# Performance work log

Measured on AMD Instinct MI355X. Metric: run time of the kernel, lower is better.

The kernel has to match this reference:

```python
import jax, jax.numpy as jnp
import numpy as np

B, L, H, U = 4, 1024, 16, 64  # batch, length, num_heads, units (per-head dim)
D_IN = 1024                   # input feature dim
D_MODEL = H * U               # 1024


def setup_inputs() -> dict:
    key = jax.random.key(0)
    ks = jax.random.split(key, 12)
    s_in = 1.0 / np.sqrt(D_IN)
    s_md = 1.0 / np.sqrt(D_MODEL)
    return {
        "v": jax.random.normal(ks[0], (B, L, D_IN), jnp.float32),
        "k": jax.random.normal(ks[1], (B, L, D_IN), jnp.float32),
        "q": jax.random.normal(ks[2], (B, L, D_IN), jnp.float32),
        "wq": jax.random.normal(ks[3], (D_IN, D_MODEL), jnp.float32) * s_in,
        "bq": jnp.zeros((D_MODEL,), jnp.float32),
        "wk": jax.random.normal(ks[4], (D_IN, D_MODEL), jnp.float32) * s_in,
        "bk": jnp.zeros((D_MODEL,), jnp.float32),
        "wv": jax.random.normal(ks[5], (D_IN, D_MODEL), jnp.float32) * s_in,
        "bv": jnp.zeros((D_MODEL,), jnp.float32),
        "wo": jax.random.normal(ks[6], (D_MODEL, U), jnp.float32) * s_md,  # dense: units*num_heads -> units
        "bo": jnp.zeros((U,), jnp.float32),
    }


def _split_heads(x):
    # (B, L, H*U) -> (B, H, L, U)
    return x.reshape(B, L, H, U).transpose(0, 2, 1, 3)


def reference(v, k, q, wq, bq, wk, bk, wv, bv, wo, bo):
    qh = _split_heads(q @ wq + bq)
    kh = _split_heads(k @ wk + bk)
    vh = _split_heads(v @ wv + bv)
    scale = 1.0 / jnp.sqrt(jnp.asarray(U, jnp.float32))
    logits = jnp.einsum("bhqd,bhkd->bhqk", qh, kh) * scale
    attn = jax.nn.softmax(logits, axis=-1)  # (B, H, Lq, Lk)
    ctx = jnp.einsum("bhqk,bhkd->bhqd", attn, vh)
    concat = ctx.transpose(0, 2, 1, 3).reshape(B, L, D_MODEL)
    out = concat @ wo + bo  # (B, L, U)
    return out, attn
```

## Files before the change

kernel.cpp:

```cpp
#include <hip/hip_runtime.h>
#include <hip/hip_bf16.h>


typedef __attribute__((ext_vector_type(8))) short s8v;
typedef __attribute__((ext_vector_type(4))) float f4v;

#define MFMA16(a, b, c) __builtin_amdgcn_mfma_f32_16x16x32_bf16(a, b, c, 0, 0, 0)

__device__ __forceinline__ ushort f2bf(float x) {
    unsigned u = __float_as_uint(x);
    return (ushort)((u + 0x7FFF + ((u >> 16) & 1)) >> 16);
}
__device__ __forceinline__ void split2(float x, ushort& h, ushort& l) {
    h = f2bf(x);
    float hf = __uint_as_float(((unsigned)h) << 16);
    l = f2bf(x - hf);
}

__global__ __launch_bounds__(256) void pack_wt(const float* __restrict__ W,
                                               ushort* __restrict__ Wt_hi,
                                               ushort* __restrict__ Wt_lo) {
    __shared__ float tile[32][36];
    const int t = threadIdx.x;
    const int n0 = blockIdx.x * 32, k0 = blockIdx.y * 32;
    {
        const int kr = t >> 3, c4 = (t & 7) * 4;
        float4 v = *(const float4*)&W[(size_t)(k0 + kr) * 1024 + n0 + c4];
        *(float4*)&tile[kr][c4] = v;
    }
    __syncthreads();
    {
        const int n = t >> 3, k4 = (t & 7) * 4;
        ushort4 h, l;
        split2(tile[k4 + 0][n], h.x, l.x);
        split2(tile[k4 + 1][n], h.y, l.y);
        split2(tile[k4 + 2][n], h.z, l.z);
        split2(tile[k4 + 3][n], h.w, l.w);
        *(ushort4*)&Wt_hi[(size_t)(n0 + n) * 1024 + k0 + k4] = h;
        *(ushort4*)&Wt_lo[(size_t)(n0 + n) * 1024 + k0 + k4] = l;
    }
}

#define PROJ_LDSTRIDE 40
template <bool SPLIT>
__global__ __launch_bounds__(256, 2) void gemm_proj_mfma(
    const float* __restrict__ X, const ushort* __restrict__ Wt_hi,
    const ushort* __restrict__ Wt_lo, const float* __restrict__ bias,
    ushort* __restrict__ Yhi, ushort* __restrict__ Ylo) {
    __shared__ ushort As_hi[128 * PROJ_LDSTRIDE];
    __shared__ ushort As_lo[128 * PROJ_LDSTRIDE];
    __shared__ ushort Bs_hi[128 * PROJ_LDSTRIDE];
    __shared__ ushort Bs_lo[128 * PROJ_LDSTRIDE];

    const int t = threadIdx.x;
    const int lane = t & 63, w = t >> 6;
    const int wm = (w & 1) * 64, wn = (w >> 1) * 64;
    const int fr = lane & 15, q8 = (lane >> 4) * 8;
    const int row0 = blockIdx.y * 128, col0 = blockIdx.x * 128;

    const int srow = t >> 1, skb = (t & 1) * 16;

    f4v acc[4][4] = {};

    for (int k0 = 0; k0 < 1024; k0 += 32) {
        {
            const float* xp = &X[(size_t)(row0 + srow) * 1024 + k0 + skb];
#pragma unroll
            for (int j = 0; j < 4; ++j) {
                float4 x4 = *(const float4*)&xp[4 * j];
                ushort4 h, l;
                split2(x4.x, h.x, l.x);
                split2(x4.y, h.y, l.y);
                split2(x4.z, h.z, l.z);
                split2(x4.w, h.w, l.w);
                *(ushort4*)&As_hi[srow * PROJ_LDSTRIDE + skb + 4 * j] = h;
                if (SPLIT) *(ushort4*)&As_lo[srow * PROJ_LDSTRIDE + skb + 4 * j] = l;
            }
        }
        {
            const ushort* bp = &Wt_hi[(size_t)(col0 + srow) * 1024 + k0 + skb];
            *(uint4*)&Bs_hi[srow * PROJ_LDSTRIDE + skb] = *(const uint4*)bp;
            *(uint4*)&Bs_hi[srow * PROJ_LDSTRIDE + skb + 8] = *(const uint4*)(bp + 8);
            if (SPLIT) {
                const ushort* bl = &Wt_lo[(size_t)(col0 + srow) * 1024 + k0 + skb];
                *(uint4*)&Bs_lo[srow * PROJ_LDSTRIDE + skb] = *(const uint4*)bl;
                *(uint4*)&Bs_lo[srow * PROJ_LDSTRIDE + skb + 8] = *(const uint4*)(bl + 8);
            }
        }
        __syncthreads();

        s8v a_hi[4], a_lo[4], b_hi[4], b_lo[4];
#pragma unroll
        for (int mi = 0; mi < 4; ++mi) {
            a_hi[mi] = *(const s8v*)&As_hi[(wm + mi * 16 + fr) * PROJ_LDSTRIDE + q8];
            if (SPLIT) a_lo[mi] = *(const s8v*)&As_lo[(wm + mi * 16 + fr) * PROJ_LDSTRIDE + q8];
        }
#pragma unroll
        for (int ni = 0; ni < 4; ++ni) {
            b_hi[ni] = *(const s8v*)&Bs_hi[(wn + ni * 16 + fr) * PROJ_LDSTRIDE + q8];
            if (SPLIT) b_lo[ni] = *(const s8v*)&Bs_lo[(wn + ni * 16 + fr) * PROJ_LDSTRIDE + q8];
        }
#pragma unroll
        for (int mi = 0; mi < 4; ++mi)
#pragma unroll
            for (int ni = 0; ni < 4; ++ni) {
                acc[mi][ni] = MFMA16(a_hi[mi], b_hi[ni], acc[mi][ni]);
                if (SPLIT) {
                    acc[mi][ni] = MFMA16(a_hi[mi], b_lo[ni], acc[mi][ni]);
                    acc[mi][ni] = MFMA16(a_lo[mi], b_hi[ni], acc[mi][ni]);
                }
            }
        __syncthreads();
    }

#pragma unroll
    for (int mi = 0; mi < 4; ++mi)
#pragma unroll
        for (int ni = 0; ni < 4; ++ni)
#pragma unroll
            for (int r = 0; r < 4; ++r) {
                const int lr = wm + mi * 16 + (lane >> 4) * 4 + r;
                const int lc = wn + ni * 16 + fr;
                const int grow = row0 + lr;
                const int b = grow >> 10, ll = grow & 1023;
                const int gcol = col0 + lc;
                const int h = gcol >> 6, u = gcol & 63;
                const float val = acc[mi][ni][r] + bias[gcol];
                const size_t o = ((size_t)((b * 16 + h) * 1024 + ll)) * 64 + u;
                if (SPLIT) {
                    ushort hh, lll;
                    split2(val, hh, lll);
                    Yhi[o] = hh;
                    Ylo[o] = lll;
                } else {
                    Yhi[o] = f2bf(val);
                }
            }
}

__global__ __launch_bounds__(256) void trans_vh(const ushort* __restrict__ vh,
                                                ushort* __restrict__ vhT) {
    __shared__ ushort st[64][72];
    const int t = threadIdx.x;
    const int bh = blockIdx.y, l0 = blockIdx.x * 64;
    {
        const int l = t >> 2, uc = (t & 3) * 16;
        const ushort* src = &vh[((size_t)bh * 1024 + l0 + l) * 64 + uc];
        *(uint4*)&st[l][uc] = *(const uint4*)src;
        *(uint4*)&st[l][uc + 8] = *(const uint4*)(src + 8);
    }
    __syncthreads();
    {
        const int u = t >> 2, lc = (t & 3) * 16;
        ushort tmp[16];
#pragma unroll
        for (int i = 0; i < 16; ++i) tmp[i] = st[lc + i][u];
        ushort* dst = &vhT[((size_t)bh * 64 + u) * 1024 + l0 + lc];
        *(uint4*)dst = *(uint4*)&tmp[0];
        *(uint4*)(dst + 8) = *(uint4*)&tmp[8];
    }
}

__device__ __forceinline__ int pswz(int row, int b) {
    return row * 2048 + (b ^ ((row & 7) << 4) ^ ((row & 8) << 2));
}

__global__ __launch_bounds__(256, 4) void attn_fused(
    const ushort* __restrict__ qh_hi, const ushort* __restrict__ qh_lo,
    const ushort* __restrict__ kh_hi, const ushort* __restrict__ kh_lo,
    const ushort* __restrict__ vhT, float* __restrict__ attn,
    float* __restrict__ ctx) {
    __shared__ ushort Pl[16 * 1024];
    __shared__ float redA[4][16];
    __shared__ float redB[4][16];

    const int t = threadIdx.x, lane = t & 63, w = t >> 6;
    const int bid = blockIdx.x;
    const int sbid = (bid & 7) * 512 + (bid >> 3);
    const int bh = sbid >> 6, q0 = (sbid & 63) * 16;
    const int fr = lane & 15, g = lane >> 4, q8 = g * 8;
    const size_t hbase = (size_t)bh * 1024 * 64;

    const ushort* qp = &qh_hi[hbase + (size_t)(q0 + fr) * 64];
    const ushort* ql = &qh_lo[hbase + (size_t)(q0 + fr) * 64];
    const s8v qb_h0 = *(const s8v*)(qp + q8), qb_h1 = *(const s8v*)(qp + 32 + q8);
    const s8v qb_l0 = *(const s8v*)(ql + q8), qb_l1 = *(const s8v*)(ql + 32 + q8);

    f4v lg[16];
#pragma unroll
    for (int i = 0; i < 16; ++i) {
        const int nt = 2 * w + 8 * (i >> 1) + (i & 1);
        const ushort* kp = &kh_hi[hbase + (size_t)(nt * 16 + fr) * 64];
        const ushort* kl = &kh_lo[hbase + (size_t)(nt * 16 + fr) * 64];
        const s8v ka_h0 = *(const s8v*)(kp + q8), ka_h1 = *(const s8v*)(kp + 32 + q8);
        const s8v ka_l0 = *(const s8v*)(kl + q8), ka_l1 = *(const s8v*)(kl + 32 + q8);
        f4v a0 = {}, a1 = {}, a2 = {};
        a0 = MFMA16(ka_h0, qb_h0, a0);
        a0 = MFMA16(ka_h1, qb_h1, a0);
        a1 = MFMA16(ka_l0, qb_h0, a1);
        a1 = MFMA16(ka_l1, qb_h1, a1);
        a2 = MFMA16(ka_h0, qb_l0, a2);
        a2 = MFMA16(ka_h1, qb_l1, a2);
#pragma unroll
        for (int r = 0; r < 4; ++r) lg[i][r] = (a0[r] + a1[r] + a2[r]) * 0.125f;
    }

    f4v mv = lg[0];
#pragma unroll
    for (int i = 1; i < 16; ++i) {
#pragma unroll
        for (int r = 0; r < 4; ++r) mv[r] = fmaxf(mv[r], lg[i][r]);
    }
    float m = fmaxf(fmaxf(mv[0], mv[1]), fmaxf(mv[2], mv[3]));
    m = fmaxf(m, __shfl_xor(m, 16));
    m = fmaxf(m, __shfl_xor(m, 32));
    if (lane < 16) redA[w][lane] = m;
    __syncthreads();
    const float m4 = fmaxf(fmaxf(redA[0][fr], redA[1][fr]),
                           fmaxf(redA[2][fr], redA[3][fr]));

    f4v sv = {0.f, 0.f, 0.f, 0.f};
#pragma unroll
    for (int i = 0; i < 16; ++i) {
#pragma unroll
        for (int r = 0; r < 4; ++r) {
            const float e = __expf(lg[i][r] - m4);
            lg[i][r] = e;
            sv[r] += e;
        }
    }
    float s = (sv[0] + sv[1]) + (sv[2] + sv[3]);
    s += __shfl_xor(s, 16);
    s += __shfl_xor(s, 32);
    if (lane < 16) redB[w][lane] = s;
    __syncthreads();
    const float inv = 1.0f / (redB[0][fr] + redB[1][fr] + redB[2][fr] + redB[3][fr]);

    char* Pb = (char*)Pl;
    float* abase = attn + ((size_t)bh << 20) + (size_t)(q0 + fr) * 1024;
#pragma unroll
    for (int j = 0; j < 8; ++j) {
        const int ntA = 2 * w + 8 * j, ntB = ntA + 1;
        const int iA = 2 * j, iB = 2 * j + 1;
        const int colA = ntA * 16 + 4 * g, colB = ntB * 16 + 4 * g;
        float4 pA, pB;
        pA.x = lg[iA][0] * inv; pA.y = lg[iA][1] * inv;
        pA.z = lg[iA][2] * inv; pA.w = lg[iA][3] * inv;
        pB.x = lg[iB][0] * inv; pB.y = lg[iB][1] * inv;
        pB.z = lg[iB][2] * inv; pB.w = lg[iB][3] * inv;
        *(float4*)&abase[colA] = pA;
        *(float4*)&abase[colB] = pB;
        ushort4 bA, bB;
        bA.x = f2bf(pA.x); bA.y = f2bf(pA.y); bA.z = f2bf(pA.z); bA.w = f2bf(pA.w);
        bB.x = f2bf(pB.x); bB.y = f2bf(pB.y); bB.z = f2bf(pB.z); bB.w = f2bf(pB.w);
        *(ushort4*)(Pb + pswz(fr, colA * 2)) = bA;
        *(ushort4*)(Pb + pswz(fr, colB * 2)) = bB;
    }
    __syncthreads();

    f4v cacc = {};
    const ushort* vp = &vhT[hbase + (size_t)(w * 16 + fr) * 1024];
#pragma unroll 4
    for (int ks = 0; ks < 32; ++ks) {
        const s8v a = *(const s8v*)(Pb + pswz(fr, ks * 64 + q8 * 2));
        const s8v b = *(const s8v*)(vp + ks * 32 + q8);
        cacc = MFMA16(a, b, cacc);
    }
#pragma unroll
    for (int r = 0; r < 4; ++r)
        ctx[((size_t)bh * 1024 + q0 + 4 * g + r) * 64 + w * 16 + fr] = cacc[r];
}

#define LDS_PAD 68
__global__ __launch_bounds__(256) void gemm_out(const float* __restrict__ ctx,
                                                const float* __restrict__ wo,
                                                const float* __restrict__ bo,
                                                float* __restrict__ out) {
    __shared__ float As[16][LDS_PAD];
    __shared__ float Bs[16][LDS_PAD];
    const int t = threadIdx.x;
    const int tx = t & 15, ty = t >> 4;
    const int row0 = blockIdx.y * 64;

    const int am = t >> 2, ak4 = t & 3;
    const int bk = t >> 4, bn4 = t & 15;

    float acc[4][4] = {};
    for (int k0 = 0; k0 < 1024; k0 += 16) {
        const int r = row0 + am;
        const int b = r >> 10, l = r & 1023;
        const int c = k0 + ak4 * 4;
        const int h = c >> 6, d = c & 63;
        float4 a = *(const float4*)&ctx[(size_t)((b * 16 + h) * 1024 + l) * 64 + d];
        float4 bvv = *(const float4*)&wo[(size_t)(k0 + bk) * 64 + bn4 * 4];
        As[ak4 * 4 + 0][am] = a.x; As[ak4 * 4 + 1][am] = a.y;
        As[ak4 * 4 + 2][am] = a.z; As[ak4 * 4 + 3][am] = a.w;
        Bs[bk][bn4 * 4 + 0] = bvv.x; Bs[bk][bn4 * 4 + 1] = bvv.y;
        Bs[bk][bn4 * 4 + 2] = bvv.z; Bs[bk][bn4 * 4 + 3] = bvv.w;
        __syncthreads();
#pragma unroll
        for (int kk = 0; kk < 16; ++kk) {
            float av[4], bv[4];
#pragma unroll
            for (int i = 0; i < 4; ++i) av[i] = As[kk][ty * 4 + i];
#pragma unroll
            for (int j = 0; j < 4; ++j) bv[j] = Bs[kk][tx * 4 + j];
#pragma unroll
            for (int i = 0; i < 4; ++i)
#pragma unroll
                for (int j = 0; j < 4; ++j) acc[i][j] += av[i] * bv[j];
        }
        __syncthreads();
    }
#pragma unroll
    for (int i = 0; i < 4; ++i) {
        const int r = row0 + ty * 4 + i;
#pragma unroll
        for (int j = 0; j < 4; ++j) {
            const int u = tx * 4 + j;
            out[(size_t)r * 64 + u] = acc[i][j] + bo[u];
        }
    }
}

extern "C" void kernel_launch(void* const* d_in, const int* in_sizes, int n_in,
                              void* d_out, int out_size, void* d_ws, size_t ws_size,
                              hipStream_t stream) {
    const float* v_in = (const float*)d_in[0];
    const float* k_in = (const float*)d_in[1];
    const float* q_in = (const float*)d_in[2];
    const float* wq = (const float*)d_in[3];
    const float* bq = (const float*)d_in[4];
    const float* wk = (const float*)d_in[5];
    const float* bk = (const float*)d_in[6];
    const float* wv = (const float*)d_in[7];
    const float* bv = (const float*)d_in[8];
    const float* wo = (const float*)d_in[9];
    const float* bo = (const float*)d_in[10];

    float* out = (float*)d_out;
    float* attn = out + 262144;

    char* w8 = (char*)d_ws;
    const size_t MB = 1u << 20;
    ushort* wtq_hi = (ushort*)(w8 + 0 * MB);
    ushort* wtq_lo = (ushort*)(w8 + 2 * MB);
    ushort* wtk_hi = (ushort*)(w8 + 4 * MB);
    ushort* wtk_lo = (ushort*)(w8 + 6 * MB);
    ushort* wtv_hi = (ushort*)(w8 + 8 * MB);
    ushort* wtv_lo = (ushort*)(w8 + 10 * MB);
    ushort* qh_hi = (ushort*)(w8 + 12 * MB);
    ushort* qh_lo = (ushort*)(w8 + 20 * MB);
    ushort* kh_hi = (ushort*)(w8 + 28 * MB);
    ushort* kh_lo = (ushort*)(w8 + 36 * MB);
    ushort* vh_hi = (ushort*)(w8 + 44 * MB);
    ushort* vh_lo = (ushort*)(w8 + 52 * MB);
    ushort* vhT = (ushort*)(w8 + 60 * MB);
    float* ctx = (float*)(w8 + 68 * MB);

    dim3 blk(256);
    pack_wt<<<dim3(32, 32), blk, 0, stream>>>(wq, wtq_hi, wtq_lo);
    pack_wt<<<dim3(32, 32), blk, 0, stream>>>(wk, wtk_hi, wtk_lo);
    pack_wt<<<dim3(32, 32), blk, 0, stream>>>(wv, wtv_hi, wtv_lo);

    gemm_proj_mfma<true><<<dim3(8, 32), blk, 0, stream>>>(q_in, wtq_hi, wtq_lo, bq, qh_hi, qh_lo);
    gemm_proj_mfma<true><<<dim3(8, 32), blk, 0, stream>>>(k_in, wtk_hi, wtk_lo, bk, kh_hi, kh_lo);
    gemm_proj_mfma<false><<<dim3(8, 32), blk, 0, stream>>>(v_in, wtv_hi, wtv_lo, bv, vh_hi, vh_lo);

    trans_vh<<<dim3(16, 64), blk, 0, stream>>>(vh_hi, vhT);

    attn_fused<<<dim3(4096), blk, 0, stream>>>(qh_hi, qh_lo, kh_hi, kh_lo, vhT, attn, ctx);

    gemm_out<<<dim3(1, 64), blk, 0, stream>>>(ctx, wo, bo, out);
}
```

Before: 735.0 us.

## Merge QKV pack/projection launches, prefetch K/V fragments, widen output GEMM grid

Merges the three weight-pack kernels and the three projection GEMMs into single launches indexed by blockIdx.z, so each step fills more of the GPU and pays one launch cost. In attention, K and V^T fragments are double-buffered in registers so the next load overlaps the current MFMAs, and the occupancy hint drops from 4 to 3 blocks to make room for the extra registers. The output GEMM is re-tiled from 64 blocks to 256 blocks, each computing 4 columns per thread, to use more CUs. Lower occupancy in the attention kernel could offset the latency hiding from prefetching.

```diff
diff --git a/kernel.cpp b/kernel.cpp
--- a/kernel.cpp
+++ b/kernel.cpp
@@ -17,9 +17,16 @@
     l = f2bf(x - hf);
 }
 
-__global__ __launch_bounds__(256) void pack_wt(const float* __restrict__ W,
-                                               ushort* __restrict__ Wt_hi,
-                                               ushort* __restrict__ Wt_lo) {
+__global__ __launch_bounds__(256) void pack_wt_all(
+    const float* __restrict__ Wq, const float* __restrict__ Wk,
+    const float* __restrict__ Wv, ushort* __restrict__ Hq,
+    ushort* __restrict__ Lq, ushort* __restrict__ Hk, ushort* __restrict__ Lk,
+    ushort* __restrict__ Hv, ushort* __restrict__ Lv) {
+    const int z = blockIdx.z;
+    const float* W = (z == 0) ? Wq : (z == 1) ? Wk : Wv;
+    ushort* WH = (z == 0) ? Hq : (z == 1) ? Hk : Hv;
+    ushort* WL = (z == 0) ? Lq : (z == 1) ? Lk : Lv;
+
     __shared__ float tile[32][36];
     const int t = threadIdx.x;
     const int n0 = blockIdx.x * 32, k0 = blockIdx.y * 32;
@@ -36,22 +43,19 @@
         split2(tile[k4 + 1][n], h.y, l.y);
         split2(tile[k4 + 2][n], h.z, l.z);
         split2(tile[k4 + 3][n], h.w, l.w);
-        *(ushort4*)&Wt_hi[(size_t)(n0 + n) * 1024 + k0 + k4] = h;
-        *(ushort4*)&Wt_lo[(size_t)(n0 + n) * 1024 + k0 + k4] = l;
+        *(ushort4*)&WH[(size_t)(n0 + n) * 1024 + k0 + k4] = h;
+        *(ushort4*)&WL[(size_t)(n0 + n) * 1024 + k0 + k4] = l;
     }
 }
 
 #define PROJ_LDSTRIDE 40
 template <bool SPLIT>
-__global__ __launch_bounds__(256, 2) void gemm_proj_mfma(
+__device__ __forceinline__ void proj_body(
+    ushort* __restrict__ As_hi, ushort* __restrict__ As_lo,
+    ushort* __restrict__ Bs_hi, ushort* __restrict__ Bs_lo,
     const float* __restrict__ X, const ushort* __restrict__ Wt_hi,
     const ushort* __restrict__ Wt_lo, const float* __restrict__ bias,
     ushort* __restrict__ Yhi, ushort* __restrict__ Ylo) {
-    __shared__ ushort As_hi[128 * PROJ_LDSTRIDE];
-    __shared__ ushort As_lo[128 * PROJ_LDSTRIDE];
-    __shared__ ushort Bs_hi[128 * PROJ_LDSTRIDE];
-    __shared__ ushort Bs_lo[128 * PROJ_LDSTRIDE];
-
     const int t = threadIdx.x;
     const int lane = t & 63, w = t >> 6;
     const int wm = (w & 1) * 64, wn = (w >> 1) * 64;
@@ -138,6 +142,32 @@
             }
 }
 
+__global__ __launch_bounds__(256, 2) void gemm_proj_all(
+    const float* __restrict__ q_in, const float* __restrict__ k_in,
+    const float* __restrict__ v_in, const ushort* __restrict__ wtq_hi,
+    const ushort* __restrict__ wtq_lo, const ushort* __restrict__ wtk_hi,
+    const ushort* __restrict__ wtk_lo, const ushort* __restrict__ wtv_hi,
+    const ushort* __restrict__ wtv_lo, const float* __restrict__ bq,
+    const float* __restrict__ bk, const float* __restrict__ bv,
+    ushort* __restrict__ qh_hi, ushort* __restrict__ qh_lo,
+    ushort* __restrict__ kh_hi, ushort* __restrict__ kh_lo,
+    ushort* __restrict__ vh_hi, ushort* __restrict__ vh_lo) {
+    __shared__ ushort As_hi[128 * PROJ_LDSTRIDE];
+    __shared__ ushort As_lo[128 * PROJ_LDSTRIDE];
+    __shared__ ushort Bs_hi[128 * PROJ_LDSTRIDE];
+    __shared__ ushort Bs_lo[128 * PROJ_LDSTRIDE];
+    const int z = blockIdx.z;
+    if (z == 0)
+        proj_body<true>(As_hi, As_lo, Bs_hi, Bs_lo, q_in, wtq_hi, wtq_lo, bq,
+                        qh_hi, qh_lo);
+    else if (z == 1)
+        proj_body<true>(As_hi, As_lo, Bs_hi, Bs_lo, k_in, wtk_hi, wtk_lo, bk,
+                        kh_hi, kh_lo);
+    else
+        proj_body<false>(As_hi, As_lo, Bs_hi, Bs_lo, v_in, wtv_hi, wtv_lo, bv,
+                         vh_hi, vh_lo);
+}
+
 __global__ __launch_bounds__(256) void trans_vh(const ushort* __restrict__ vh,
                                                 ushort* __restrict__ vhT) {
     __shared__ ushort st[64][72];
@@ -165,7 +195,7 @@
     return row * 2048 + (b ^ ((row & 7) << 4) ^ ((row & 8) << 2));
 }
 
-__global__ __launch_bounds__(256, 4) void attn_fused(
+__global__ __launch_bounds__(256, 3) void attn_fused(
     const ushort* __restrict__ qh_hi, const ushort* __restrict__ qh_lo,
     const ushort* __restrict__ kh_hi, const ushort* __restrict__ kh_lo,
     const ushort* __restrict__ vhT, float* __restrict__ attn,
@@ -186,21 +216,37 @@
     const s8v qb_h0 = *(const s8v*)(qp + q8), qb_h1 = *(const s8v*)(qp + 32 + q8);
     const s8v qb_l0 = *(const s8v*)(ql + q8), qb_l1 = *(const s8v*)(ql + 32 + q8);
 
+    auto kofs = [&](int i) {
+        const int nt = 2 * w + 8 * (i >> 1) + (i & 1);
+        return hbase + (size_t)(nt * 16 + fr) * 64;
+    };
+
     f4v lg[16];
+    s8v kh0[2], kh1[2], kl0[2], kl1[2];
+    {
+        const size_t o0 = kofs(0);
+        kh0[0] = *(const s8v*)(kh_hi + o0 + q8);
+        kh1[0] = *(const s8v*)(kh_hi + o0 + 32 + q8);
+        kl0[0] = *(const s8v*)(kh_lo + o0 + q8);
+        kl1[0] = *(const s8v*)(kh_lo + o0 + 32 + q8);
+    }
 #pragma unroll
     for (int i = 0; i < 16; ++i) {
-        const int nt = 2 * w + 8 * (i >> 1) + (i & 1);
-        const ushort* kp = &kh_hi[hbase + (size_t)(nt * 16 + fr) * 64];
-        const ushort* kl = &kh_lo[hbase + (size_t)(nt * 16 + fr) * 64];
-        const s8v ka_h0 = *(const s8v*)(kp + q8), ka_h1 = *(const s8v*)(kp + 32 + q8);
-        const s8v ka_l0 = *(const s8v*)(kl + q8), ka_l1 = *(const s8v*)(kl + 32 + q8);
+        const int cur = i & 1, nxt = cur ^ 1;
+        if (i < 15) {
+            const size_t on = kofs(i + 1);
+            kh0[nxt] = *(const s8v*)(kh_hi + on + q8);
+            kh1[nxt] = *(const s8v*)(kh_hi + on + 32 + q8);
+            kl0[nxt] = *(const s8v*)(kh_lo + on + q8);
+            kl1[nxt] = *(const s8v*)(kh_lo + on + 32 + q8);
+        }
         f4v a0 = {}, a1 = {}, a2 = {};
-        a0 = MFMA16(ka_h0, qb_h0, a0);
-        a0 = MFMA16(ka_h1, qb_h1, a0);
-        a1 = MFMA16(ka_l0, qb_h0, a1);
-        a1 = MFMA16(ka_l1, qb_h1, a1);
-        a2 = MFMA16(ka_h0, qb_l0, a2);
-        a2 = MFMA16(ka_h1, qb_l1, a2);
+        a0 = MFMA16(kh0[cur], qb_h0, a0);
+        a0 = MFMA16(kh1[cur], qb_h1, a0);
+        a1 = MFMA16(kl0[cur], qb_h0, a1);
+        a1 = MFMA16(kl1[cur], qb_h1, a1);
+        a2 = MFMA16(kh0[cur], qb_l0, a2);
+        a2 = MFMA16(kh1[cur], qb_l1, a2);
 #pragma unroll
         for (int r = 0; r < 4; ++r) lg[i][r] = (a0[r] + a1[r] + a2[r]) * 0.125f;
     }
@@ -240,9 +286,9 @@
     float* abase = attn + ((size_t)bh << 20) + (size_t)(q0 + fr) * 1024;
 #pragma unroll
     for (int j = 0; j < 8; ++j) {
-        const int ntA = 2 * w + 8 * j, ntB = ntA + 1;
         const int iA = 2 * j, iB = 2 * j + 1;
-        const int colA = ntA * 16 + 4 * g, colB = ntB * 16 + 4 * g;
+        const int ntA = 2 * w + 8 * j;
+        const int colA = ntA * 16 + 4 * g, colB = colA + 16;
         float4 pA, pB;
         pA.x = lg[iA][0] * inv; pA.y = lg[iA][1] * inv;
         pA.z = lg[iA][2] * inv; pA.w = lg[iA][3] * inv;
@@ -260,67 +306,63 @@
 
     f4v cacc = {};
     const ushort* vp = &vhT[hbase + (size_t)(w * 16 + fr) * 1024];
-#pragma unroll 4
+    s8v vb[2];
+    vb[0] = *(const s8v*)(vp + q8);
+#pragma unroll
     for (int ks = 0; ks < 32; ++ks) {
+        const int cur = ks & 1, nxt = cur ^ 1;
+        if (ks < 31) vb[nxt] = *(const s8v*)(vp + (ks + 1) * 32 + q8);
         const s8v a = *(const s8v*)(Pb + pswz(fr, ks * 64 + q8 * 2));
-        const s8v b = *(const s8v*)(vp + ks * 32 + q8);
-        cacc = MFMA16(a, b, cacc);
+        cacc = MFMA16(a, vb[cur], cacc);
     }
 #pragma unroll
     for (int r = 0; r < 4; ++r)
         ctx[((size_t)bh * 1024 + q0 + 4 * g + r) * 64 + w * 16 + fr] = cacc[r];
 }
 
-#define LDS_PAD 68
 __global__ __launch_bounds__(256) void gemm_out(const float* __restrict__ ctx,
                                                 const float* __restrict__ wo,
                                                 const float* __restrict__ bo,
                                                 float* __restrict__ out) {
-    __shared__ float As[16][LDS_PAD];
-    __shared__ float Bs[16][LDS_PAD];
+    __shared__ float As[16][68];
+    __shared__ float Bs[16][20];
     const int t = threadIdx.x;
-    const int tx = t & 15, ty = t >> 4;
+    const int row = t >> 2, c4 = (t & 3) * 4;
+    const int n0 = blockIdx.x * 16;
     const int row0 = blockIdx.y * 64;
 
     const int am = t >> 2, ak4 = t & 3;
-    const int bk = t >> 4, bn4 = t & 15;
-
-    float acc[4][4] = {};
+
+    float acc[4] = {};
     for (int k0 = 0; k0 < 1024; k0 += 16) {
-        const int r = row0 + am;
-        const int b = r >> 10, l = r & 1023;
-        const int c = k0 + ak4 * 4;
-        const int h = c >> 6, d = c & 63;
-        float4 a = *(const float4*)&ctx[(size_t)((b * 16 + h) * 1024 + l) * 64 + d];
-        float4 bvv = *(const float4*)&wo[(size_t)(k0 + bk) * 64 + bn4 * 4];
-        As[ak4 * 4 + 0][am] = a.x; As[ak4 * 4 + 1][am] = a.y;
-        As[ak4 * 4 + 2][am] = a.z; As[ak4 * 4 + 3][am] = a.w;
-        Bs[bk][bn4 * 4 + 0] = bvv.x; Bs[bk][bn4 * 4 + 1] = bvv.y;
-        Bs[bk][bn4 * 4 + 2] = bvv.z; Bs[bk][bn4 * 4 + 3] = bvv.w;
+        {
+            const int r = row0 + am;
+            const int b = r >> 10, l = r & 1023;
+            const int c = k0 + ak4 * 4;
+            const int h = c >> 6, d = c & 63;
+            float4 a = *(const float4*)&ctx[(size_t)((b * 16 + h) * 1024 + l) * 64 + d];
+            As[ak4 * 4 + 0][am] = a.x; As[ak4 * 4 + 1][am] = a.y;
+            As[ak4 * 4 + 2][am] = a.z; As[ak4 * 4 + 3][am] = a.w;
+        }
+        if (t < 64) {
+            const int bk = t >> 2, bc4 = (t & 3) * 4;
+            float4 bv = *(const float4*)&wo[(size_t)(k0 + bk) * 64 + n0 + bc4];
+            Bs[bk][bc4 + 0] = bv.x; Bs[bk][bc4 + 1] = bv.y;
+            Bs[bk][bc4 + 2] = bv.z; Bs[bk][bc4 + 3] = bv.w;
+        }
         __syncthreads();
 #pragma unroll
         for (int kk = 0; kk < 16; ++kk) {
-            float av[4], bv[4];
-#pragma unroll
-            for (int i = 0; i < 4; ++i) av[i] = As[kk][ty * 4 + i];
-#pragma unroll
-            for (int j = 0; j < 4; ++j) bv[j] = Bs[kk][tx * 4 + j];
-#pragma unroll
-            for (int i = 0; i < 4; ++i)
-#pragma unroll
-                for (int j = 0; j < 4; ++j) acc[i][j] += av[i] * bv[j];
+            const float a = As[kk][row];
+            const float4 bv = *(const float4*)&Bs[kk][c4];
+            acc[0] += a * bv.x; acc[1] += a * bv.y;
+            acc[2] += a * bv.z; acc[3] += a * bv.w;
         }
         __syncthreads();
     }
 #pragma unroll
-    for (int i = 0; i < 4; ++i) {
-        const int r = row0 + ty * 4 + i;
-#pragma unroll
-        for (int j = 0; j < 4; ++j) {
-            const int u = tx * 4 + j;
-            out[(size_t)r * 64 + u] = acc[i][j] + bo[u];
-        }
-    }
+    for (int j = 0; j < 4; ++j)
+        out[(size_t)(row0 + row) * 64 + n0 + c4 + j] = acc[j] + bo[n0 + c4 + j];
 }
 
 extern "C" void kernel_launch(void* const* d_in, const int* in_sizes, int n_in,
@@ -358,18 +400,17 @@
     ushort* vhT = (ushort*)(w8 + 60 * MB);
     float* ctx = (float*)(w8 + 68 * MB);
 
-    dim3 blk(256);
-    pack_wt<<<dim3(32, 32), blk, 0, stream>>>(wq, wtq_hi, wtq_lo);
-    pack_wt<<<dim3(32, 32), blk, 0, stream>>>(wk, wtk_hi, wtk_lo);
-    pack_wt<<<dim3(32, 32), blk, 0, stream>>>(wv, wtv_hi, wtv_lo);
-
-    gemm_proj_mfma<true><<<dim3(8, 32), blk, 0, stream>>>(q_in, wtq_hi, wtq_lo, bq, qh_hi, qh_lo);
-    gemm_proj_mfma<true><<<dim3(8, 32), blk, 0, stream>>>(k_in, wtk_hi, wtk_lo, bk, kh_hi, kh_lo);
-    gemm_proj_mfma<false><<<dim3(8, 32), blk, 0, stream>>>(v_in, wtv_hi, wtv_lo, bv, vh_hi, vh_lo);
-
-    trans_vh<<<dim3(16, 64), blk, 0, stream>>>(vh_hi, vhT);
-
-    attn_fused<<<dim3(4096), blk, 0, stream>>>(qh_hi, qh_lo, kh_hi, kh_lo, vhT, attn, ctx);
-
-    gemm_out<<<dim3(1, 64), blk, 0, stream>>>(ctx, wo, bo, out);
-}
+    pack_wt_all<<<dim3(32, 32, 3), dim3(256), 0, stream>>>(
+        wq, wk, wv, wtq_hi, wtq_lo, wtk_hi, wtk_lo, wtv_hi, wtv_lo);
+
+    gemm_proj_all<<<dim3(8, 32, 3), dim3(256), 0, stream>>>(
+        q_in, k_in, v_in, wtq_hi, wtq_lo, wtk_hi, wtk_lo, wtv_hi, wtv_lo,
+        bq, bk, bv, qh_hi, qh_lo, kh_hi, kh_lo, vh_hi, vh_lo);
+
+    trans_vh<<<dim3(16, 64), dim3(256), 0, stream>>>(vh_hi, vhT);
+
+    attn_fused<<<dim3(4096), dim3(256), 0, stream>>>(qh_hi, qh_lo, kh_hi, kh_lo,
+                                                     vhT, attn, ctx);
+
+    gemm_out<<<dim3(4, 64), dim3(256), 0, stream>>>(ctx, wo, bo, out);
+}
```

Measured after the change: 626.3 us. 14.8% less time.
